# Kernel tuning notes

Hardware: AMD Instinct MI355X
Metric: run time of the kernel (lower is better)

The kernel has to match this reference:

```python
import jax, jax.numpy as jnp
import numpy as np

D_MODEL = 1024
H = 16
DK = D_MODEL // H
D_FC = 4096
B = 2
S = 1024
EPS = 1e-6


def setup_inputs() -> dict:
    key = jax.random.key(0)
    ks = jax.random.split(key, 8)
    sc = 1.0 / np.sqrt(D_MODEL)
    return {
        "x": jax.random.normal(ks[0], (B, S, D_MODEL), dtype=jnp.float32),
        "mask": jnp.ones((B, 1, 1, S), dtype=jnp.int32),
        "w_q": jax.random.normal(ks[1], (D_MODEL, D_MODEL), dtype=jnp.float32) * sc,
        "w_k": jax.random.normal(ks[2], (D_MODEL, D_MODEL), dtype=jnp.float32) * sc,
        "w_v": jax.random.normal(ks[3], (D_MODEL, D_MODEL), dtype=jnp.float32) * sc,
        "w_o": jax.random.normal(ks[4], (D_MODEL, D_MODEL), dtype=jnp.float32) * sc,
        "alpha1": jnp.ones((D_MODEL,), dtype=jnp.float32),
        "beta1": jnp.zeros((D_MODEL,), dtype=jnp.float32),
        "alpha2": jnp.ones((D_MODEL,), dtype=jnp.float32),
        "beta2": jnp.zeros((D_MODEL,), dtype=jnp.float32),
        "fc1_w": jax.random.normal(ks[5], (D_FC, D_MODEL), dtype=jnp.float32) * sc,
        "fc1_b": jnp.zeros((D_FC,), dtype=jnp.float32),
        "fc2_w": jax.random.normal(ks[6], (D_MODEL, D_FC), dtype=jnp.float32) * (1.0 / np.sqrt(D_FC)),
        "fc2_b": jnp.zeros((D_MODEL,), dtype=jnp.float32),
    }


def _layernorm(x, alpha, beta):
    # Matches torch: mean and std (unbiased, ddof=1), divide by (std + eps)
    mean = jnp.mean(x, axis=-1, keepdims=True)
    std = jnp.std(x, axis=-1, keepdims=True, ddof=1)
    return alpha * (x - mean) / (std + EPS) + beta


def _mha(x, mask, w_q, w_k, w_v, w_o):
    # nn.Linear(bias=False): y = x @ W.T
    q = (x @ w_q.T).reshape(B, S, H, DK).transpose(0, 2, 1, 3)  # (B,H,S,DK)
    k = (x @ w_k.T).reshape(B, S, H, DK).transpose(0, 2, 1, 3)
    v = (x @ w_v.T).reshape(B, S, H, DK).transpose(0, 2, 1, 3)
    scores = jnp.einsum('bhqd,bhkd->bhqk', q, k) / jnp.sqrt(jnp.float32(DK))
    scores = jnp.where(mask == 0, jnp.float32(-1e9), scores)
    attn = jax.nn.softmax(scores, axis=-1)  # dropout=0 (eval)
    out = jnp.einsum('bhqk,bhkd->bhqd', attn, v)  # (B,H,S,DK)
    out = out.transpose(0, 2, 1, 3).reshape(B, S, D_MODEL)
    return out @ w_o.T


def _ffn(x, fc1_w, fc1_b, fc2_w, fc2_b):
    h = jax.nn.relu(x @ fc1_w.T + fc1_b)
    return h @ fc2_w.T + fc2_b


def reference(x, mask, w_q, w_k, w_v, w_o, alpha1, beta1, alpha2, beta2,
              fc1_w, fc1_b, fc2_w, fc2_b):
    # Pre-LN residual block 1: attention
    x = x + _mha(_layernorm(x, alpha1, beta1), mask, w_q, w_k, w_v, w_o)
    # Pre-LN residual block 2: FFN
    x = x + _ffn(_layernorm(x, alpha2, beta2), fc1_w, fc1_b, fc2_w, fc2_b)
    return x
```

## Files before the change

### kernel.cpp

```cpp
#include <hip/hip_runtime.h>
#include <hip/hip_bf16.h>


typedef __bf16 bf16;
typedef __attribute__((ext_vector_type(8))) __bf16 bf16x8;
typedef __attribute__((ext_vector_type(4))) __bf16 bf16x4;
typedef __attribute__((ext_vector_type(4))) float f32x4;

#define NTOK 2048
#define DM   1024
#define DFC  4096
#define QKVN 3072

__device__ inline void gl_lds16(const void* g, void* l) {
    __builtin_amdgcn_global_load_lds((const __attribute__((address_space(1))) void*)g,
                                     (__attribute__((address_space(3))) void*)l, 16, 0, 0);
}

__device__ inline void ln_row(float4 v, const float* alpha, const float* beta,
                              bf16* outrow, int t) {
    float s  = v.x + v.y + v.z + v.w;
    float ss = v.x * v.x + v.y * v.y + v.z * v.z + v.w * v.w;
    __shared__ float red[8];
    int lane = t & 63, wv = t >> 6;
    #pragma unroll
    for (int o = 32; o > 0; o >>= 1) {
        s  += __shfl_down(s, o);
        ss += __shfl_down(ss, o);
    }
    if (lane == 0) { red[wv] = s; red[4 + wv] = ss; }
    __syncthreads();
    float S  = red[0] + red[1] + red[2] + red[3];
    float SS = red[4] + red[5] + red[6] + red[7];
    float mean = S * (1.0f / 1024.0f);
    float var  = (SS - S * mean) * (1.0f / 1023.0f);
    var = var < 0.f ? 0.f : var;
    float inv = 1.0f / (sqrtf(var) + 1e-6f);
    float4 a4 = reinterpret_cast<const float4*>(alpha)[t];
    float4 b4 = reinterpret_cast<const float4*>(beta)[t];
    bf16x4 o4;
    o4[0] = (bf16)(a4.x * (v.x - mean) * inv + b4.x);
    o4[1] = (bf16)(a4.y * (v.y - mean) * inv + b4.y);
    o4[2] = (bf16)(a4.z * (v.z - mean) * inv + b4.z);
    o4[3] = (bf16)(a4.w * (v.w - mean) * inv + b4.w);
    reinterpret_cast<bf16x4*>(outrow)[t] = o4;
}

__global__ __launch_bounds__(256) void prep_kernel(
    const float4* __restrict__ wq, const float4* __restrict__ wk,
    const float4* __restrict__ wv, const float4* __restrict__ wo,
    const float4* __restrict__ f1, const float4* __restrict__ f2,
    bf16x4* __restrict__ oqkv, bf16x4* __restrict__ oo,
    bf16x4* __restrict__ of1, bf16x4* __restrict__ of2,
    const float* __restrict__ x, const float* __restrict__ alpha1,
    const float* __restrict__ beta1, bf16* __restrict__ xn) {
    int blk = blockIdx.x;
    int t = threadIdx.x;
    if (blk < 12288) {
        int i = blk * 256 + t;
        const int Q = 262144;
        float4 v;
        bf16x4* dst;
        if (i < 3 * Q) {
            v = (i < Q) ? wq[i] : (i < 2 * Q) ? wk[i - Q] : wv[i - 2 * Q];
            dst = oqkv + i;
        } else if (i < 4 * Q) {
            v = wo[i - 3 * Q];
            dst = oo + (i - 3 * Q);
        } else if (i < 8 * Q) {
            v = f1[i - 4 * Q];
            dst = of1 + (i - 4 * Q);
        } else {
            v = f2[i - 8 * Q];
            dst = of2 + (i - 8 * Q);
        }
        bf16x4 o;
        o[0] = (bf16)v.x; o[1] = (bf16)v.y; o[2] = (bf16)v.z; o[3] = (bf16)v.w;
        *dst = o;
    } else {
        int row = blk - 12288;
        float4 v = reinterpret_cast<const float4*>(x + (size_t)row * DM)[t];
        ln_row(v, alpha1, beta1, xn + (size_t)row * DM, t);
    }
}

__global__ __launch_bounds__(256) void reduce_ln_kernel(const float* __restrict__ p,
                                                        const float* __restrict__ resid,
                                                        const float* __restrict__ alpha,
                                                        const float* __restrict__ beta,
                                                        float* __restrict__ x2,
                                                        bf16* __restrict__ xn) {
    int row = blockIdx.x, t = threadIdx.x;
    size_t i4 = (size_t)row * 256 + t;
    float4 a = reinterpret_cast<const float4*>(p)[i4];
    float4 b = reinterpret_cast<const float4*>(p)[i4 + 524288];
    float4 r = reinterpret_cast<const float4*>(resid)[i4];
    float4 v;
    v.x = a.x + b.x + r.x; v.y = a.y + b.y + r.y;
    v.z = a.z + b.z + r.z; v.w = a.w + b.w + r.w;
    reinterpret_cast<float4*>(x2)[i4] = v;
    ln_row(v, alpha, beta, xn + (size_t)row * DM, t);
}

__global__ __launch_bounds__(256) void reduce_out_kernel(const float* __restrict__ p,
                                                         const float* __restrict__ bias,
                                                         const float* __restrict__ x2,
                                                         float* __restrict__ out) {
    size_t i4 = (size_t)blockIdx.x * 256 + threadIdx.x;
    float4 a = reinterpret_cast<const float4*>(p)[i4];
    float4 b = reinterpret_cast<const float4*>(p)[i4 + 524288];
    float4 r = reinterpret_cast<const float4*>(x2)[i4];
    float4 bi = reinterpret_cast<const float4*>(bias)[i4 & 255];
    float4 o;
    o.x = a.x + b.x + r.x + bi.x; o.y = a.y + b.y + r.y + bi.y;
    o.z = a.z + b.z + r.z + bi.z; o.w = a.w + b.w + r.w + bi.w;
    reinterpret_cast<float4*>(out)[i4] = o;
}

template <int EPI>
__global__ __launch_bounds__(256) void gemm128(const bf16* __restrict__ A,
                                               const bf16* __restrict__ Bt,
                                               void* __restrict__ outp,
                                               const float* __restrict__ bias,
                                               int M, int N, int K, int kslice) {
    __shared__ bf16 As[2][128 * 64];
    __shared__ bf16 Bs[2][128 * 64];
    int tid = threadIdx.x;
    int lane = tid & 63, wave = tid >> 6;
    int q = lane >> 4, r = lane & 15;
    int wm = wave >> 1, wn = wave & 1;
    int m0 = blockIdx.y * 128, n0 = blockIdx.x * 128;
    int kbeg = blockIdx.z * kslice;
    int nit = kslice / 64;
    f32x4 acc[4][4] = {};

    int srow = tid >> 3;
    int csrc = (tid & 7) ^ (srow & 7);
    const bf16* agp = A  + (size_t)(m0 + srow) * K + kbeg + csrc * 8;
    const bf16* bgp = Bt + (size_t)(n0 + srow) * K + kbeg + csrc * 8;

    int rsw = (r & 7);
    int co0 = ((q ^ rsw) * 8);
    int co1 = co0 ^ 32;
    int aoff = (wm * 64 + r) * 64;
    int boff = (wn * 64 + r) * 64;

    auto stage = [&](int it, int b) {
        int k0 = it * 64;
        #pragma unroll
        for (int j = 0; j < 4; ++j) {
            gl_lds16(agp + (size_t)j * 32 * K + k0, &As[b][tid * 8 + j * 2048]);
            gl_lds16(bgp + (size_t)j * 32 * K + k0, &Bs[b][tid * 8 + j * 2048]);
        }
    };

    stage(0, 0);
    for (int it = 0; it < nit; ++it) {
        __syncthreads();
        if (it + 1 < nit) stage(it + 1, (it + 1) & 1);
        const bf16* Ab = &As[it & 1][aoff];
        const bf16* Bb = &Bs[it & 1][boff];
        #pragma unroll
        for (int half = 0; half < 2; ++half) {
            int co = half ? co1 : co0;
            bf16x8 af[4], bfv[4];
            #pragma unroll
            for (int t = 0; t < 4; ++t)
                af[t] = *reinterpret_cast<const bf16x8*>(Ab + t * 1024 + co);
            #pragma unroll
            for (int u = 0; u < 4; ++u)
                bfv[u] = *reinterpret_cast<const bf16x8*>(Bb + u * 1024 + co);
            #pragma unroll
            for (int t = 0; t < 4; ++t)
                #pragma unroll
                for (int u = 0; u < 4; ++u)
                    acc[t][u] = __builtin_amdgcn_mfma_f32_16x16x32_bf16(af[t], bfv[u], acc[t][u], 0, 0, 0);
        }
    }

    size_t zoff = (size_t)blockIdx.z * M * N;
    #pragma unroll
    for (int t = 0; t < 4; ++t) {
        #pragma unroll
        for (int u = 0; u < 4; ++u) {
            #pragma unroll
            for (int i = 0; i < 4; ++i) {
                int mm = m0 + wm * 64 + t * 16 + q * 4 + i;
                int nn = n0 + wn * 64 + u * 16 + r;
                size_t idx = (size_t)mm * N + nn;
                float v = acc[t][u][i];
                if (EPI == 0) {
                    ((bf16*)outp)[idx] = (bf16)v;
                } else if (EPI == 1) {
                    v += bias[nn];
                    ((bf16*)outp)[idx] = (bf16)(v > 0.f ? v : 0.f);
                } else {
                    ((float*)outp)[zoff + idx] = v;
                }
            }
        }
    }
}

__global__ void transpose_v(const bf16* __restrict__ qkv, bf16* __restrict__ vt) {
    __shared__ bf16 tile[32][33];
    int bh = blockIdx.z;
    int b = bh >> 4, h = bh & 15;
    int s0 = blockIdx.x * 32;
    int d0 = blockIdx.y * 32;
    int tx = threadIdx.x, ty = threadIdx.y;
    tile[ty][tx] = qkv[(size_t)(b * 1024 + s0 + ty) * QKVN + 2048 + h * 64 + d0 + tx];
    __syncthreads();
    vt[(size_t)(bh * 64 + d0 + ty) * 1024 + s0 + tx] = tile[tx][ty];
}

__global__ __launch_bounds__(256) void attn_kernel(const bf16* __restrict__ qkv,
                                                   const bf16* __restrict__ Vt,
                                                   const int* __restrict__ mask,
                                                   bf16* __restrict__ out) {
    __shared__ bf16 Ks[2][4096];
    __shared__ bf16 Vs[2][4096];
    __shared__ bf16 pbuf[4][1024];
    __shared__ float msk[1024];
    int tid = threadIdx.x;
    int lane = tid & 63, w = tid >> 6;
    int q = lane >> 4, r = lane & 15;
    int id = blockIdx.x;
    int qb = id & 15, h = (id >> 4) & 15, b = id >> 8;

    {
        int4 mi = reinterpret_cast<const int4*>(mask + b * 1024)[tid];
        msk[tid * 4 + 0] = mi.x ? 0.f : -1e9f;
        msk[tid * 4 + 1] = mi.y ? 0.f : -1e9f;
        msk[tid * 4 + 2] = mi.z ? 0.f : -1e9f;
        msk[tid * 4 + 3] = mi.w ? 0.f : -1e9f;
    }

    const bf16* qrow = qkv + (size_t)(b * 1024 + qb * 64 + w * 16 + r) * QKVN + h * 64 + q * 8;
    bf16x8 qf0 = *reinterpret_cast<const bf16x8*>(qrow);
    bf16x8 qf1 = *reinterpret_cast<const bf16x8*>(qrow + 32);

    int csw = (tid & 7) ^ ((tid >> 3) & 7);
    const bf16* kg0 = qkv + (size_t)(b * 1024 + (tid >> 3)) * QKVN + 1024 + h * 64 + csw * 8;
    const bf16* kg1 = kg0 + (size_t)32 * QKVN;
    const bf16* vg0 = Vt + (size_t)((b * 16 + h) * 64 + (tid >> 3)) * 1024 + csw * 8;
    const bf16* vg1 = vg0 + 32 * 1024;
    bf16* kld = &Ks[0][tid * 8];
    bf16* vld = &Vs[0][tid * 8];

    int co0 = (q ^ (r & 7)) * 8;
    bf16* pw = pbuf[w];

    float m[4] = {-1e30f, -1e30f, -1e30f, -1e30f};
    float l[4] = {0.f, 0.f, 0.f, 0.f};
    f32x4 o[4] = {};

    gl_lds16(kg0, kld);
    gl_lds16(kg1, kld + 2048);
    gl_lds16(vg0, vld);
    gl_lds16(vg1, vld + 2048);

    for (int t = 0; t < 16; ++t) {
        __syncthreads();
        if (t < 15) {
            int ktn = (t + 1) * 64;
            int bo = ((t + 1) & 1) * 4096;
            gl_lds16(kg0 + (size_t)ktn * QKVN, kld + bo);
            gl_lds16(kg1 + (size_t)ktn * QKVN, kld + bo + 2048);
            gl_lds16(vg0 + ktn, vld + bo);
            gl_lds16(vg1 + ktn, vld + bo + 2048);
        }
        const bf16* Kb = Ks[t & 1];
        const bf16* Vb = Vs[t & 1];
        int kt = t * 64;

        f32x4 s[4];
        #pragma unroll
        for (int ks = 0; ks < 4; ++ks) {
            bf16x8 kf0 = *reinterpret_cast<const bf16x8*>(&Kb[(ks * 16 + r) * 64 + co0]);
            bf16x8 kf1 = *reinterpret_cast<const bf16x8*>(&Kb[(ks * 16 + r) * 64 + (co0 ^ 32)]);
            f32x4 a = {};
            a = __builtin_amdgcn_mfma_f32_16x16x32_bf16(qf0, kf0, a, 0, 0, 0);
            a = __builtin_amdgcn_mfma_f32_16x16x32_bf16(qf1, kf1, a, 0, 0, 0);
            float mb = msk[kt + ks * 16 + r];
            #pragma unroll
            for (int i = 0; i < 4; ++i) s[ks][i] = fmaf(a[i], 0.125f, mb);
        }
        float alpha[4];
        #pragma unroll
        for (int i = 0; i < 4; ++i) {
            float t2 = fmaxf(fmaxf(s[0][i], s[1][i]), fmaxf(s[2][i], s[3][i]));
            t2 = fmaxf(t2, __shfl_xor(t2, 1));
            t2 = fmaxf(t2, __shfl_xor(t2, 2));
            t2 = fmaxf(t2, __shfl_xor(t2, 4));
            t2 = fmaxf(t2, __shfl_xor(t2, 8));
            float mn = fmaxf(m[i], t2);
            alpha[i] = __expf(m[i] - mn);
            m[i] = mn;
        }
        #pragma unroll
        for (int i = 0; i < 4; ++i) {
            float e0 = __expf(s[0][i] - m[i]);
            float e1 = __expf(s[1][i] - m[i]);
            float e2 = __expf(s[2][i] - m[i]);
            float e3 = __expf(s[3][i] - m[i]);
            s[0][i] = e0; s[1][i] = e1; s[2][i] = e2; s[3][i] = e3;
            float rs = (e0 + e1) + (e2 + e3);
            rs += __shfl_xor(rs, 1);
            rs += __shfl_xor(rs, 2);
            rs += __shfl_xor(rs, 4);
            rs += __shfl_xor(rs, 8);
            l[i] = l[i] * alpha[i] + rs;
        }
        #pragma unroll
        for (int nt = 0; nt < 4; ++nt)
            #pragma unroll
            for (int i = 0; i < 4; ++i) o[nt][i] *= alpha[i];
        #pragma unroll
        for (int ks = 0; ks < 4; ++ks) {
            int kc = ks * 2 + (r >> 3);
            #pragma unroll
            for (int i = 0; i < 4; ++i) {
                int mr = q * 4 + i;
                pw[mr * 64 + ((kc ^ (mr & 7)) * 8) + (r & 7)] = (bf16)s[ks][i];
            }
        }
        #pragma unroll
        for (int ks2 = 0; ks2 < 2; ++ks2) {
            int vpo = (((ks2 * 4 + q) ^ (r & 7)) * 8);
            bf16x8 pf = *reinterpret_cast<const bf16x8*>(&pw[r * 64 + vpo]);
            #pragma unroll
            for (int nt = 0; nt < 4; ++nt) {
                bf16x8 vf = *reinterpret_cast<const bf16x8*>(&Vb[(nt * 16 + r) * 64 + vpo]);
                o[nt] = __builtin_amdgcn_mfma_f32_16x16x32_bf16(pf, vf, o[nt], 0, 0, 0);
            }
        }
    }

    float inv[4];
    #pragma unroll
    for (int i = 0; i < 4; ++i) inv[i] = 1.0f / l[i];
    #pragma unroll
    for (int nt = 0; nt < 4; ++nt)
        #pragma unroll
        for (int i = 0; i < 4; ++i)
            out[(size_t)(b * 1024 + qb * 64 + w * 16 + q * 4 + i) * DM + h * 64 + nt * 16 + r] =
                (bf16)(o[nt][i] * inv[i]);
}

extern "C" void kernel_launch(void* const* d_in, const int* in_sizes, int n_in,
                              void* d_out, int out_size, void* d_ws, size_t ws_size,
                              hipStream_t stream) {
    const float* x      = (const float*)d_in[0];
    const int*   mask   = (const int*)  d_in[1];
    const float* w_q    = (const float*)d_in[2];
    const float* w_k    = (const float*)d_in[3];
    const float* w_v    = (const float*)d_in[4];
    const float* w_o    = (const float*)d_in[5];
    const float* alpha1 = (const float*)d_in[6];
    const float* beta1  = (const float*)d_in[7];
    const float* alpha2 = (const float*)d_in[8];
    const float* beta2  = (const float*)d_in[9];
    const float* fc1_w  = (const float*)d_in[10];
    const float* fc1_b  = (const float*)d_in[11];
    const float* fc2_w  = (const float*)d_in[12];
    const float* fc2_b  = (const float*)d_in[13];
    float* out = (float*)d_out;

    char* ws = (char*)d_ws;
    const size_t MB = 1024 * 1024;
    bf16*  wqkv_b = (bf16*)(ws +  0 * MB);
    bf16*  wo_b   = (bf16*)(ws +  6 * MB);
    bf16*  f1w_b  = (bf16*)(ws +  8 * MB);
    bf16*  f2w_b  = (bf16*)(ws + 16 * MB);
    bf16*  xn     = (bf16*)(ws + 24 * MB);
    bf16*  qkvb   = (bf16*)(ws + 28 * MB);
    bf16*  vtb    = (bf16*)(ws + 40 * MB);
    bf16*  attnb  = (bf16*)(ws + 44 * MB);
    float* x2     = (float*)(ws + 48 * MB);
    float* po     = (float*)(ws + 28 * MB);
    bf16*  hb     = (bf16*)(ws + 28 * MB);
    float* pf2    = (float*)(ws +  0 * MB);

    prep_kernel<<<14336, 256, 0, stream>>>(
        (const float4*)w_q, (const float4*)w_k, (const float4*)w_v, (const float4*)w_o,
        (const float4*)fc1_w, (const float4*)fc2_w,
        (bf16x4*)wqkv_b, (bf16x4*)wo_b, (bf16x4*)f1w_b, (bf16x4*)f2w_b,
        x, alpha1, beta1, xn);

    gemm128<0><<<dim3(QKVN / 128, NTOK / 128, 1), 256, 0, stream>>>(
        xn, wqkv_b, qkvb, nullptr, NTOK, QKVN, DM, DM);

    transpose_v<<<dim3(32, 2, 32), dim3(32, 32), 0, stream>>>(qkvb, vtb);

    attn_kernel<<<512, 256, 0, stream>>>(qkvb, vtb, mask, attnb);

    gemm128<4><<<dim3(DM / 128, NTOK / 128, 2), 256, 0, stream>>>(
        attnb, wo_b, po, nullptr, NTOK, DM, DM, DM / 2);

    reduce_ln_kernel<<<NTOK, 256, 0, stream>>>(po, x, alpha2, beta2, x2, xn);

    gemm128<1><<<dim3(DFC / 128, NTOK / 128, 1), 256, 0, stream>>>(
        xn, f1w_b, hb, fc1_b, NTOK, DFC, DM, DM);

    gemm128<4><<<dim3(DM / 128, NTOK / 128, 2), 256, 0, stream>>>(
        hb, f2w_b, pf2, nullptr, NTOK, DM, DFC, DFC / 2);

    reduce_out_kernel<<<2048, 256, 0, stream>>>(pf2, fc2_b, x2, out);
}
```

Before: 262.7 us.

## Shrink GEMM tiles to 128x64 with BK=32 and compute softmax row sums via MFMA

Replaces the 128x128x64 GEMM tile with a 128x64 tile and a 32-wide K step, doubling the grid so the 256-CU device gets more blocks for each of the four projection GEMMs. It also uses less LDS per block, which may allow more blocks per CU. Separately, the attention kernel drops the shuffle-based row-sum reduction and instead accumulates the softmax denominator with an extra MFMA against a vector of ones. That sum is now taken over bf16-rounded probabilities. The cost is lower reuse per tile, more synchronisation steps per K, and a slight change in numerics.

```diff
diff --git a/kernel.cpp b/kernel.cpp
--- a/kernel.cpp
+++ b/kernel.cpp
@@ -118,40 +118,37 @@
 }
 
 template <int EPI>
-__global__ __launch_bounds__(256) void gemm128(const bf16* __restrict__ A,
-                                               const bf16* __restrict__ Bt,
-                                               void* __restrict__ outp,
-                                               const float* __restrict__ bias,
-                                               int M, int N, int K, int kslice) {
-    __shared__ bf16 As[2][128 * 64];
-    __shared__ bf16 Bs[2][128 * 64];
+__global__ __launch_bounds__(256) void gemm64(const bf16* __restrict__ A,
+                                              const bf16* __restrict__ Bt,
+                                              void* __restrict__ outp,
+                                              const float* __restrict__ bias,
+                                              int M, int N, int K, int kslice) {
+    __shared__ bf16 As[2][128 * 32];
+    __shared__ bf16 Bs[2][64 * 32];
     int tid = threadIdx.x;
-    int lane = tid & 63, wave = tid >> 6;
+    int lane = tid & 63, w = tid >> 6;
     int q = lane >> 4, r = lane & 15;
-    int wm = wave >> 1, wn = wave & 1;
-    int m0 = blockIdx.y * 128, n0 = blockIdx.x * 128;
+    int wm = w >> 1, wn = w & 1;
+    int m0 = blockIdx.y * 128, n0 = blockIdx.x * 64;
     int kbeg = blockIdx.z * kslice;
-    int nit = kslice / 64;
-    f32x4 acc[4][4] = {};
-
-    int srow = tid >> 3;
-    int csrc = (tid & 7) ^ (srow & 7);
-    const bf16* agp = A  + (size_t)(m0 + srow) * K + kbeg + csrc * 8;
-    const bf16* bgp = Bt + (size_t)(n0 + srow) * K + kbeg + csrc * 8;
-
-    int rsw = (r & 7);
-    int co0 = ((q ^ rsw) * 8);
-    int co1 = co0 ^ 32;
-    int aoff = (wm * 64 + r) * 64;
-    int boff = (wn * 64 + r) * 64;
+    int nit = kslice / 32;
+    f32x4 acc[4][2] = {};
+
+    int csrc = (lane & 3) ^ ((lane >> 3) & 3);
+    int srow = w * 16 + (lane >> 2);
+    const bf16* agp0 = A  + (size_t)(m0 + srow) * K + kbeg + csrc * 8;
+    const bf16* agp1 = A  + (size_t)(m0 + 64 + srow) * K + kbeg + csrc * 8;
+    const bf16* bgp  = Bt + (size_t)(n0 + srow) * K + kbeg + csrc * 8;
+
+    int pos = (q ^ ((r >> 1) & 3)) * 8;
+    int aoff = (wm * 64 + r) * 32 + pos;
+    int boff = (wn * 32 + r) * 32 + pos;
 
     auto stage = [&](int it, int b) {
-        int k0 = it * 64;
-        #pragma unroll
-        for (int j = 0; j < 4; ++j) {
-            gl_lds16(agp + (size_t)j * 32 * K + k0, &As[b][tid * 8 + j * 2048]);
-            gl_lds16(bgp + (size_t)j * 32 * K + k0, &Bs[b][tid * 8 + j * 2048]);
-        }
+        int k0 = it * 32;
+        gl_lds16(agp0 + k0, &As[b][w * 512 + lane * 8]);
+        gl_lds16(agp1 + k0, &As[b][(w + 4) * 512 + lane * 8]);
+        gl_lds16(bgp  + k0, &Bs[b][w * 512 + lane * 8]);
     };
 
     stage(0, 0);
@@ -160,33 +157,29 @@
         if (it + 1 < nit) stage(it + 1, (it + 1) & 1);
         const bf16* Ab = &As[it & 1][aoff];
         const bf16* Bb = &Bs[it & 1][boff];
-        #pragma unroll
-        for (int half = 0; half < 2; ++half) {
-            int co = half ? co1 : co0;
-            bf16x8 af[4], bfv[4];
+        bf16x8 af[4], bfv[2];
+        #pragma unroll
+        for (int t = 0; t < 4; ++t)
+            af[t] = *reinterpret_cast<const bf16x8*>(Ab + t * 512);
+        #pragma unroll
+        for (int u = 0; u < 2; ++u)
+            bfv[u] = *reinterpret_cast<const bf16x8*>(Bb + u * 512);
+        #pragma unroll
+        for (int t = 0; t < 4; ++t)
             #pragma unroll
-            for (int t = 0; t < 4; ++t)
-                af[t] = *reinterpret_cast<const bf16x8*>(Ab + t * 1024 + co);
-            #pragma unroll
-            for (int u = 0; u < 4; ++u)
-                bfv[u] = *reinterpret_cast<const bf16x8*>(Bb + u * 1024 + co);
-            #pragma unroll
-            for (int t = 0; t < 4; ++t)
-                #pragma unroll
-                for (int u = 0; u < 4; ++u)
-                    acc[t][u] = __builtin_amdgcn_mfma_f32_16x16x32_bf16(af[t], bfv[u], acc[t][u], 0, 0, 0);
-        }
+            for (int u = 0; u < 2; ++u)
+                acc[t][u] = __builtin_amdgcn_mfma_f32_16x16x32_bf16(af[t], bfv[u], acc[t][u], 0, 0, 0);
     }
 
     size_t zoff = (size_t)blockIdx.z * M * N;
     #pragma unroll
     for (int t = 0; t < 4; ++t) {
         #pragma unroll
-        for (int u = 0; u < 4; ++u) {
+        for (int u = 0; u < 2; ++u) {
             #pragma unroll
             for (int i = 0; i < 4; ++i) {
                 int mm = m0 + wm * 64 + t * 16 + q * 4 + i;
-                int nn = n0 + wn * 64 + u * 16 + r;
+                int nn = n0 + wn * 32 + u * 16 + r;
                 size_t idx = (size_t)mm * N + nn;
                 float v = acc[t][u][i];
                 if (EPI == 0) {
@@ -250,9 +243,12 @@
 
     int co0 = (q ^ (r & 7)) * 8;
     bf16* pw = pbuf[w];
+    bf16x8 ones;
+    #pragma unroll
+    for (int j = 0; j < 8; ++j) ones[j] = (bf16)1.0f;
 
     float m[4] = {-1e30f, -1e30f, -1e30f, -1e30f};
-    float l[4] = {0.f, 0.f, 0.f, 0.f};
+    f32x4 osum = {};
     f32x4 o[4] = {};
 
     gl_lds16(kg0, kld);
@@ -300,22 +296,17 @@
         }
         #pragma unroll
         for (int i = 0; i < 4; ++i) {
-            float e0 = __expf(s[0][i] - m[i]);
-            float e1 = __expf(s[1][i] - m[i]);
-            float e2 = __expf(s[2][i] - m[i]);
-            float e3 = __expf(s[3][i] - m[i]);
-            s[0][i] = e0; s[1][i] = e1; s[2][i] = e2; s[3][i] = e3;
-            float rs = (e0 + e1) + (e2 + e3);
-            rs += __shfl_xor(rs, 1);
-            rs += __shfl_xor(rs, 2);
-            rs += __shfl_xor(rs, 4);
-            rs += __shfl_xor(rs, 8);
-            l[i] = l[i] * alpha[i] + rs;
-        }
-        #pragma unroll
-        for (int nt = 0; nt < 4; ++nt)
-            #pragma unroll
-            for (int i = 0; i < 4; ++i) o[nt][i] *= alpha[i];
+            s[0][i] = __expf(s[0][i] - m[i]);
+            s[1][i] = __expf(s[1][i] - m[i]);
+            s[2][i] = __expf(s[2][i] - m[i]);
+            s[3][i] = __expf(s[3][i] - m[i]);
+        }
+        #pragma unroll
+        for (int i = 0; i < 4; ++i) {
+            osum[i] *= alpha[i];
+            o[0][i] *= alpha[i]; o[1][i] *= alpha[i];
+            o[2][i] *= alpha[i]; o[3][i] *= alpha[i];
+        }
         #pragma unroll
         for (int ks = 0; ks < 4; ++ks) {
             int kc = ks * 2 + (r >> 3);
@@ -334,12 +325,13 @@
                 bf16x8 vf = *reinterpret_cast<const bf16x8*>(&Vb[(nt * 16 + r) * 64 + vpo]);
                 o[nt] = __builtin_amdgcn_mfma_f32_16x16x32_bf16(pf, vf, o[nt], 0, 0, 0);
             }
+            osum = __builtin_amdgcn_mfma_f32_16x16x32_bf16(pf, ones, osum, 0, 0, 0);
         }
     }
 
     float inv[4];
     #pragma unroll
-    for (int i = 0; i < 4; ++i) inv[i] = 1.0f / l[i];
+    for (int i = 0; i < 4; ++i) inv[i] = 1.0f / osum[i];
     #pragma unroll
     for (int nt = 0; nt < 4; ++nt)
         #pragma unroll
@@ -388,22 +380,22 @@
         (bf16x4*)wqkv_b, (bf16x4*)wo_b, (bf16x4*)f1w_b, (bf16x4*)f2w_b,
         x, alpha1, beta1, xn);
 
-    gemm128<0><<<dim3(QKVN / 128, NTOK / 128, 1), 256, 0, stream>>>(
+    gemm64<0><<<dim3(QKVN / 64, NTOK / 128, 1), 256, 0, stream>>>(
         xn, wqkv_b, qkvb, nullptr, NTOK, QKVN, DM, DM);
 
     transpose_v<<<dim3(32, 2, 32), dim3(32, 32), 0, stream>>>(qkvb, vtb);
 
     attn_kernel<<<512, 256, 0, stream>>>(qkvb, vtb, mask, attnb);
 
-    gemm128<4><<<dim3(DM / 128, NTOK / 128, 2), 256, 0, stream>>>(
+    gemm64<4><<<dim3(DM / 64, NTOK / 128, 2), 256, 0, stream>>>(
         attnb, wo_b, po, nullptr, NTOK, DM, DM, DM / 2);
 
     reduce_ln_kernel<<<NTOK, 256, 0, stream>>>(po, x, alpha2, beta2, x2, xn);
 
-    gemm128<1><<<dim3(DFC / 128, NTOK / 128, 1), 256, 0, stream>>>(
+    gemm64<1><<<dim3(DFC / 64, NTOK / 128, 1), 256, 0, stream>>>(
         xn, f1w_b, hb, fc1_b, NTOK, DFC, DM, DM);
 
-    gemm128<4><<<dim3(DM / 128, NTOK / 128, 2), 256, 0, stream>>>(
+    gemm64<4><<<dim3(DM / 64, NTOK / 128, 2), 256, 0, stream>>>(
         hb, f2w_b, pf2, nullptr, NTOK, DM, DFC, DFC / 2);
 
     reduce_out_kernel<<<2048, 256, 0, stream>>>(pf2, fc2_b, x2, out);
```

Result: slower. 274.8 us (+4.6%).

## Remap blocks across XCDs and compute softmax row sums with MFMA

Applied to the files above, without the earlier changes.

Remaps GEMM and attention block indices so that blocks sharing the same K/V head or B tiles land on the same XCD, which should improve L2 reuse. In attention, the per-row softmax sum is now taken by an extra MFMA of the bf16 probabilities against a ones vector, replacing the shuffle reduction. The sum is therefore built from the same rounded bf16 values used in P·V, which changes numerics slightly. The GEMM remap assumes gridDim.x is divisible by 8.

```diff
diff --git a/kernel.cpp b/kernel.cpp
--- a/kernel.cpp
+++ b/kernel.cpp
@@ -129,7 +129,15 @@
     int lane = tid & 63, wave = tid >> 6;
     int q = lane >> 4, r = lane & 15;
     int wm = wave >> 1, wn = wave & 1;
-    int m0 = blockIdx.y * 128, n0 = blockIdx.x * 128;
+
+    int lid = blockIdx.y * gridDim.x + blockIdx.x;
+    int nxp = gridDim.x >> 3;
+    int xcd = lid & 7;
+    int loc = lid >> 3;
+    int bx = xcd * nxp + (loc % nxp);
+    int by = loc / nxp;
+
+    int m0 = by * 128, n0 = bx * 128;
     int kbeg = blockIdx.z * kslice;
     int nit = kslice / 64;
     f32x4 acc[4][4] = {};
@@ -225,8 +233,12 @@
     int tid = threadIdx.x;
     int lane = tid & 63, w = tid >> 6;
     int q = lane >> 4, r = lane & 15;
+
     int id = blockIdx.x;
-    int qb = id & 15, h = (id >> 4) & 15, b = id >> 8;
+    int xcd = id & 7, j = id >> 3;
+    int bh = xcd * 4 + (j >> 4);
+    int qb = j & 15;
+    int b = bh >> 4, h = bh & 15;
 
     {
         int4 mi = reinterpret_cast<const int4*>(mask + b * 1024)[tid];
@@ -250,9 +262,12 @@
 
     int co0 = (q ^ (r & 7)) * 8;
     bf16* pw = pbuf[w];
+    bf16x8 ones;
+    #pragma unroll
+    for (int jj = 0; jj < 8; ++jj) ones[jj] = (bf16)1.0f;
 
     float m[4] = {-1e30f, -1e30f, -1e30f, -1e30f};
-    float l[4] = {0.f, 0.f, 0.f, 0.f};
+    f32x4 osum = {};
     f32x4 o[4] = {};
 
     gl_lds16(kg0, kld);
@@ -300,22 +315,17 @@
         }
         #pragma unroll
         for (int i = 0; i < 4; ++i) {
-            float e0 = __expf(s[0][i] - m[i]);
-            float e1 = __expf(s[1][i] - m[i]);
-            float e2 = __expf(s[2][i] - m[i]);
-            float e3 = __expf(s[3][i] - m[i]);
-            s[0][i] = e0; s[1][i] = e1; s[2][i] = e2; s[3][i] = e3;
-            float rs = (e0 + e1) + (e2 + e3);
-            rs += __shfl_xor(rs, 1);
-            rs += __shfl_xor(rs, 2);
-            rs += __shfl_xor(rs, 4);
-            rs += __shfl_xor(rs, 8);
-            l[i] = l[i] * alpha[i] + rs;
-        }
-        #pragma unroll
-        for (int nt = 0; nt < 4; ++nt)
-            #pragma unroll
-            for (int i = 0; i < 4; ++i) o[nt][i] *= alpha[i];
+            s[0][i] = __expf(s[0][i] - m[i]);
+            s[1][i] = __expf(s[1][i] - m[i]);
+            s[2][i] = __expf(s[2][i] - m[i]);
+            s[3][i] = __expf(s[3][i] - m[i]);
+        }
+        #pragma unroll
+        for (int i = 0; i < 4; ++i) {
+            osum[i] *= alpha[i];
+            o[0][i] *= alpha[i]; o[1][i] *= alpha[i];
+            o[2][i] *= alpha[i]; o[3][i] *= alpha[i];
+        }
         #pragma unroll
         for (int ks = 0; ks < 4; ++ks) {
             int kc = ks * 2 + (r >> 3);
@@ -334,12 +344,13 @@
                 bf16x8 vf = *reinterpret_cast<const bf16x8*>(&Vb[(nt * 16 + r) * 64 + vpo]);
                 o[nt] = __builtin_amdgcn_mfma_f32_16x16x32_bf16(pf, vf, o[nt], 0, 0, 0);
             }
+            osum = __builtin_amdgcn_mfma_f32_16x16x32_bf16(pf, ones, osum, 0, 0, 0);
         }
     }
 
     float inv[4];
     #pragma unroll
-    for (int i = 0; i < 4; ++i) inv[i] = 1.0f / l[i];
+    for (int i = 0; i < 4; ++i) inv[i] = 1.0f / osum[i];
     #pragma unroll
     for (int nt = 0; nt < 4; ++nt)
         #pragma unroll
```

Result: no change. 260.4 us (-0.9%).
